# Optimization experiments

Measured on AMD Instinct MI355X. Metric: run time of the kernel, lower is better.

## Reference

```python
import jax, jax.numpy as jnp
import numpy as np

B, S, F, H, A = 2, 2048, 1024, 16, 64


def setup_inputs() -> dict:
    key = jax.random.key(0)
    ks = jax.random.split(key, 6)
    return {
        "key_input": jax.random.normal(ks[0], (B, S, F), dtype=jnp.float32),
        "query_input": jax.random.normal(ks[1], (B, S, F), dtype=jnp.float32),
        "value_input": jax.random.normal(ks[2], (B, S, F), dtype=jnp.float32),
        "q_w": jax.random.normal(ks[3], (H, F, A), dtype=jnp.float32) * (1.0 / np.sqrt(F)),
        "k_w": jax.random.normal(ks[4], (H, F, A), dtype=jnp.float32) * (1.0 / np.sqrt(F)),
        "v_w": jax.random.normal(ks[5], (H, F, A), dtype=jnp.float32) * (1.0 / np.sqrt(F)),
    }


def reference(key_input, query_input, value_input, q_w, k_w, v_w):
    attention_len = q_w.shape[-1]
    # per-head QKV projections: [B,S,F] x [H,F,A] -> [B,S,H,A]
    keys = jnp.einsum('bsf,hfa->bsha', key_input, k_w)
    queries = jnp.einsum('bsf,hfa->bsha', query_input, q_w)
    values = jnp.einsum('bsf,hfa->bsha', value_input, v_w)
    # scores: [B,H,Q,K]; NOTE: original softmaxes over dim=2 (the query axis)
    energy = jnp.einsum('bqha,bkha->bhqk', queries, keys) / jnp.sqrt(
        jnp.asarray(attention_len, dtype=queries.dtype))
    scores = jax.nn.softmax(energy, axis=2)
    # NOTE: original einsum 'bhqs,bsha->bsha' sums over q, keeps s aligned with values
    return jnp.einsum('bhqs,bsha->bsha', scores, values)
```

## Files before the change

### kernel.cpp

```cpp
#include <hip/hip_runtime.h>
#include <hip/hip_bf16.h>

typedef __bf16 bf16_t;
typedef __bf16 bf16x4 __attribute__((ext_vector_type(4)));
typedef __bf16 bf16x8 __attribute__((ext_vector_type(8)));
typedef float  f32x4  __attribute__((ext_vector_type(4)));

typedef __attribute__((address_space(1))) const void  gvoid_t;
typedef __attribute__((address_space(3))) void        lvoid_t;

static constexpr int Mtot = 4096;
static constexpr int Ntot = 1024;
static constexpr int Ktot = 1024;


__global__ __launch_bounds__(256)
void prepass_kernel(const float* __restrict__ A, const float* __restrict__ W,
                    bf16_t* __restrict__ Ab, bf16_t* __restrict__ Wt)
{
    __shared__ float wtile[64][65];
    const int bid = blockIdx.x, t = threadIdx.x;

    if (bid < 1024) {
        const size_t base = (size_t)bid * 4096 + t * 4;
#pragma unroll
        for (int r = 0; r < 4; ++r) {
            const size_t i = base + (size_t)r * 1024;
            const f32x4 v = *(const f32x4*)(A + i);
            bf16x4 p = {(bf16_t)v[0], (bf16_t)v[1], (bf16_t)v[2], (bf16_t)v[3]};
            *(bf16x4*)(Ab + i) = p;
        }
    } else {
        const int wb = bid - 1024;
        const int head = wb >> 4;
        const int k0 = (wb & 15) * 64;
        const float* wsrc = W + (size_t)head * (Ktot * 64) + (size_t)k0 * 64;
#pragma unroll
        for (int i = 0; i < 4; ++i) {
            const int idx = i * 256 + t;
            const int kr = idx >> 4, a4 = (idx & 15) * 4;
            const f32x4 v = *(const f32x4*)(wsrc + (size_t)kr * 64 + a4);
            wtile[kr][a4 + 0] = v[0]; wtile[kr][a4 + 1] = v[1];
            wtile[kr][a4 + 2] = v[2]; wtile[kr][a4 + 3] = v[3];
        }
        __syncthreads();
#pragma unroll
        for (int i = 0; i < 4; ++i) {
            const int idx = i * 256 + t;
            const int ar = idx >> 4, kc = (idx & 15) * 4;
            bf16x4 p = {(bf16_t)wtile[kc + 0][ar], (bf16_t)wtile[kc + 1][ar],
                        (bf16_t)wtile[kc + 2][ar], (bf16_t)wtile[kc + 3][ar]};
            *(bf16x4*)(Wt + (size_t)(head * 64 + ar) * Ktot + k0 + kc) = p;
        }
    }
}

__global__ __launch_bounds__(256, 2)
void gemm_bf16_kernel(const bf16_t* __restrict__ Ab, const bf16_t* __restrict__ Bt,
                      float* __restrict__ C)
{
    __shared__ bf16_t As[2][64 * 64];
    __shared__ bf16_t Bs[2][128 * 64];

    const int t = threadIdx.x, lane = t & 63, wave = t >> 6;
    const int wm = wave & 1, wn = wave >> 1;

    const int g = (blockIdx.x & 7) * 64 + (blockIdx.x >> 3);
    const int by = g >> 3, bx = g & 7;
    const int bm = by * 64, bn = bx * 128;

    const int lrow = lane & 15;
    const int lq   = lane >> 4;

    f32x4 acc[2][4];
#pragma unroll
    for (int mf = 0; mf < 2; ++mf)
#pragma unroll
        for (int nf = 0; nf < 4; ++nf) {
            f32x4 z = {0.f, 0.f, 0.f, 0.f};
            acc[mf][nf] = z;
        }

    auto STAGE = [&](int buf, int k0) {
#pragma unroll
        for (int j = 0; j < 2; ++j) {
            const int chunk = (wave * 2 + j) * 64 + lane;
            const int row = chunk >> 3;
            const int kb  = ((chunk & 7) ^ (row & 7)) * 8;
            const bf16_t* gp = Ab + (size_t)(bm + row) * Ktot + k0 + kb;
            __builtin_amdgcn_global_load_lds((gvoid_t*)gp,
                (lvoid_t*)&As[buf][(wave * 2 + j) * 512], 16, 0, 0);
        }
#pragma unroll
        for (int j = 0; j < 4; ++j) {
            const int chunk = (wave * 4 + j) * 64 + lane;
            const int row = chunk >> 3;
            const int kb  = ((chunk & 7) ^ (row & 7)) * 8;
            const bf16_t* gp = Bt + (size_t)(bn + row) * Ktot + k0 + kb;
            __builtin_amdgcn_global_load_lds((gvoid_t*)gp,
                (lvoid_t*)&Bs[buf][(wave * 4 + j) * 512], 16, 0, 0);
        }
    };

    auto COMPUTE = [&](int cur) {
#pragma unroll
        for (int kk = 0; kk < 2; ++kk) {
            const int c16 = kk * 4 + lq;
            bf16x8 af[2], bfr[4];
#pragma unroll
            for (int mf = 0; mf < 2; ++mf) {
                const int R = wm * 32 + mf * 16 + lrow;
                af[mf] = *(const bf16x8*)&As[cur][R * 64 + ((c16 ^ (R & 7)) << 3)];
            }
#pragma unroll
            for (int nf = 0; nf < 4; ++nf) {
                const int R = wn * 64 + nf * 16 + lrow;
                bfr[nf] = *(const bf16x8*)&Bs[cur][R * 64 + ((c16 ^ (R & 7)) << 3)];
            }
            __builtin_amdgcn_s_setprio(1);
#pragma unroll
            for (int mf = 0; mf < 2; ++mf)
#pragma unroll
                for (int nf = 0; nf < 4; ++nf)
                    acc[mf][nf] = __builtin_amdgcn_mfma_f32_16x16x32_bf16(
                        af[mf], bfr[nf], acc[mf][nf], 0, 0, 0);
            __builtin_amdgcn_s_setprio(0);
        }
    };

    constexpr int NT = Ktot / 64;
    STAGE(0, 0);

    for (int tI = 0; tI < NT - 1; ++tI) {
        const int cur = tI & 1;
        __builtin_amdgcn_s_barrier();
        STAGE(cur ^ 1, (tI + 1) * 64);
        asm volatile("s_waitcnt vmcnt(6)" ::: "memory");
        __builtin_amdgcn_sched_barrier(0);
        __builtin_amdgcn_s_barrier();
        __builtin_amdgcn_sched_barrier(0);
        COMPUTE(cur);
    }
    asm volatile("s_waitcnt vmcnt(0)" ::: "memory");
    __builtin_amdgcn_sched_barrier(0);
    __builtin_amdgcn_s_barrier();
    __builtin_amdgcn_sched_barrier(0);
    COMPUTE((NT - 1) & 1);

#pragma unroll
    for (int mf = 0; mf < 2; ++mf) {
        const int row0 = bm + wm * 32 + mf * 16 + (lq << 2);
#pragma unroll
        for (int nf = 0; nf < 4; ++nf) {
            const int col = bn + wn * 64 + nf * 16 + lrow;
#pragma unroll
            for (int i = 0; i < 4; ++i)
                C[(size_t)(row0 + i) * Ntot + col] = acc[mf][nf][i];
        }
    }
}

static constexpr int FBM = 128, FBN = 128, FBK = 64, FBKP = 72;

__global__ __launch_bounds__(512, 2)
void vproj_fused_kernel(const float* __restrict__ A, const float* __restrict__ W,
                        float* __restrict__ C)
{
    __shared__ bf16_t As[2][FBM][FBKP];
    __shared__ bf16_t Bs[2][FBN][FBKP];

    const int t = threadIdx.x, lane = t & 63, wave = t >> 6;
    const int wm = wave >> 2, wn = wave & 3;
    const int tile = (blockIdx.x & 7) * 32 + (blockIdx.x >> 3);
    const int bm = (tile >> 3) * FBM, bn = (tile & 7) * FBN;

    const int bhead = t >> 8, brem = t & 255;
    const int bkq = brem >> 4, baq = brem & 15;
    const float* const wbase = W + ((size_t)((bn >> 6) + bhead)) * (Ktot * 64)
                                 + (size_t)(bkq * 4) * 64 + baq * 4;
    f32x4 avreg[4], bvreg[4];

    auto load_tile = [&](int k0) {
#pragma unroll
        for (int r = 0; r < 4; ++r) {
            const int idx = r * 512 + t;
            avreg[r] = *(const f32x4*)(A + (size_t)(bm + (idx >> 4)) * Ktot + k0 + (idx & 15) * 4);
        }
        const float* wp = wbase + (size_t)k0 * 64;
#pragma unroll
        for (int r = 0; r < 4; ++r) bvreg[r] = *(const f32x4*)(wp + r * 64);
    };
    auto store_tile = [&](int buf) {
#pragma unroll
        for (int r = 0; r < 4; ++r) {
            const int idx = r * 512 + t;
            bf16_t* dst = &As[buf][idx >> 4][(idx & 15) * 4];
            dst[0] = (bf16_t)avreg[r][0]; dst[1] = (bf16_t)avreg[r][1];
            dst[2] = (bf16_t)avreg[r][2]; dst[3] = (bf16_t)avreg[r][3];
        }
#pragma unroll
        for (int j = 0; j < 4; ++j) {
            bf16_t* dst = &Bs[buf][bhead * 64 + baq * 4 + j][bkq * 4];
            dst[0] = (bf16_t)bvreg[0][j]; dst[1] = (bf16_t)bvreg[1][j];
            dst[2] = (bf16_t)bvreg[2][j]; dst[3] = (bf16_t)bvreg[3][j];
        }
    };

    f32x4 acc[4][2];
#pragma unroll
    for (int mf = 0; mf < 4; ++mf)
#pragma unroll
        for (int nf = 0; nf < 2; ++nf) { f32x4 z = {0,0,0,0}; acc[mf][nf] = z; }

    const int lrow = lane & 15, lkb = (lane >> 4) << 3;
    load_tile(0); store_tile(0); __syncthreads();

    for (int tI = 0; tI < Ktot / FBK; ++tI) {
        const int cur = tI & 1;
        if (tI + 1 < Ktot / FBK) load_tile((tI + 1) * FBK);
#pragma unroll
        for (int kk = 0; kk < 2; ++kk) {
            bf16x8 af[4], bfr[2];
#pragma unroll
            for (int mf = 0; mf < 4; ++mf)
                af[mf] = *(const bf16x8*)&As[cur][wm * 64 + mf * 16 + lrow][kk * 32 + lkb];
#pragma unroll
            for (int nf = 0; nf < 2; ++nf)
                bfr[nf] = *(const bf16x8*)&Bs[cur][wn * 32 + nf * 16 + lrow][kk * 32 + lkb];
#pragma unroll
            for (int mf = 0; mf < 4; ++mf)
#pragma unroll
                for (int nf = 0; nf < 2; ++nf)
                    acc[mf][nf] = __builtin_amdgcn_mfma_f32_16x16x32_bf16(
                        af[mf], bfr[nf], acc[mf][nf], 0, 0, 0);
        }
        if (tI + 1 < Ktot / FBK) store_tile(cur ^ 1);
        __syncthreads();
    }
#pragma unroll
    for (int mf = 0; mf < 4; ++mf) {
        const int row0 = bm + wm * 64 + mf * 16 + ((lane >> 4) << 2);
#pragma unroll
        for (int nf = 0; nf < 2; ++nf) {
            const int col = bn + wn * 32 + nf * 16 + (lane & 15);
#pragma unroll
            for (int i = 0; i < 4; ++i)
                C[(size_t)(row0 + i) * Ntot + col] = acc[mf][nf][i];
        }
    }
}

extern "C" void kernel_launch(void* const* d_in, const int* in_sizes, int n_in,
                              void* d_out, int out_size, void* d_ws, size_t ws_size,
                              hipStream_t stream) {
    (void)in_sizes; (void)n_in; (void)out_size;
    const float* V  = (const float*)d_in[2];
    const float* Vw = (const float*)d_in[5];
    float* out      = (float*)d_out;

    const size_t abBytes = (size_t)Mtot * Ktot * sizeof(bf16_t);
    const size_t wtBytes = (size_t)Ntot * Ktot * sizeof(bf16_t);

    if (ws_size >= abBytes + wtBytes) {
        bf16_t* Ab = (bf16_t*)d_ws;
        bf16_t* Wt = (bf16_t*)((char*)d_ws + abBytes);
        hipLaunchKernelGGL(prepass_kernel, dim3(1024 + 256), dim3(256), 0, stream,
                           V, Vw, Ab, Wt);
        hipLaunchKernelGGL(gemm_bf16_kernel, dim3((Mtot / 64) * (Ntot / 128)),
                           dim3(256), 0, stream, Ab, Wt, out);
    } else {
        hipLaunchKernelGGL(vproj_fused_kernel, dim3(256), dim3(512), 0, stream,
                           V, Vw, out);
    }
}
```

Measured before the change: 30.14 us.

## Fuse bf16 prepass and GEMM into one cooperative kernel with grid sync

Merges the fp32-to-bf16 conversion/transpose prepass and the bf16 MFMA GEMM into a single cooperative kernel of 512 blocks. The blocks first convert their slice of activations and weights, then meet at a grid-wide barrier before running the GEMM. This is meant to remove the second kernel launch and the gap between the two kernels. In exchange it pays for a grid sync and requires all 512 blocks to be co-resident, with the old two-kernel path kept as a fallback when cooperative launch is unsupported.

```diff
diff --git a/kernel.cpp b/kernel.cpp
--- a/kernel.cpp
+++ b/kernel.cpp
@@ -1,5 +1,8 @@
 #include <hip/hip_runtime.h>
 #include <hip/hip_bf16.h>
+#include <hip/hip_cooperative_groups.h>
+
+namespace cg = cooperative_groups;
 
 typedef __bf16 bf16_t;
 typedef __bf16 bf16x4 __attribute__((ext_vector_type(4)));
@@ -14,29 +17,35 @@
 static constexpr int Ktot = 1024;
 
 
-__global__ __launch_bounds__(256)
-void prepass_kernel(const float* __restrict__ A, const float* __restrict__ W,
-                    bf16_t* __restrict__ Ab, bf16_t* __restrict__ Wt)
+__global__ __launch_bounds__(256, 2)
+void fused_coop_kernel(const float* __restrict__ A, const float* __restrict__ W,
+                       bf16_t* __restrict__ Ab, bf16_t* __restrict__ Wt,
+                       float* __restrict__ C)
 {
-    __shared__ float wtile[64][65];
-    const int bid = blockIdx.x, t = threadIdx.x;
-
-    if (bid < 1024) {
-        const size_t base = (size_t)bid * 4096 + t * 4;
-#pragma unroll
-        for (int r = 0; r < 4; ++r) {
-            const size_t i = base + (size_t)r * 1024;
-            const f32x4 v = *(const f32x4*)(A + i);
+    __shared__ bf16_t As[2][64 * 64];
+    __shared__ bf16_t Bs[2][128 * 64];
+
+    const int t = threadIdx.x, lane = t & 63, wave = t >> 6;
+    const int bid = blockIdx.x;
+
+    {
+        const int row0 = (bid & 7) * 512 + (bid >> 3) * 8;
+#pragma unroll
+        for (int r = 0; r < 8; ++r) {
+            const size_t off = (size_t)(row0 + r) * Ktot + t * 4;
+            const f32x4 v = *(const f32x4*)(A + off);
             bf16x4 p = {(bf16_t)v[0], (bf16_t)v[1], (bf16_t)v[2], (bf16_t)v[3]};
-            *(bf16x4*)(Ab + i) = p;
-        }
-    } else {
-        const int wb = bid - 1024;
+            *(bf16x4*)(Ab + off) = p;
+        }
+    }
+    {
+        float (*wtile)[65] = (float(*)[65])(&Bs[0][0]);
+        const int wb = bid >> 1;
         const int head = wb >> 4;
-        const int k0 = (wb & 15) * 64;
+        const int k0 = (wb & 15) * 64 + (bid & 1) * 32;
         const float* wsrc = W + (size_t)head * (Ktot * 64) + (size_t)k0 * 64;
 #pragma unroll
-        for (int i = 0; i < 4; ++i) {
+        for (int i = 0; i < 2; ++i) {
             const int idx = i * 256 + t;
             const int kr = idx >> 4, a4 = (idx & 15) * 4;
             const f32x4 v = *(const f32x4*)(wsrc + (size_t)kr * 64 + a4);
@@ -45,30 +54,21 @@
         }
         __syncthreads();
 #pragma unroll
-        for (int i = 0; i < 4; ++i) {
+        for (int i = 0; i < 2; ++i) {
             const int idx = i * 256 + t;
-            const int ar = idx >> 4, kc = (idx & 15) * 4;
+            const int ar = idx >> 3, kc = (idx & 7) * 4;
             bf16x4 p = {(bf16_t)wtile[kc + 0][ar], (bf16_t)wtile[kc + 1][ar],
                         (bf16_t)wtile[kc + 2][ar], (bf16_t)wtile[kc + 3][ar]};
             *(bf16x4*)(Wt + (size_t)(head * 64 + ar) * Ktot + k0 + kc) = p;
         }
     }
-}
-
-__global__ __launch_bounds__(256, 2)
-void gemm_bf16_kernel(const bf16_t* __restrict__ Ab, const bf16_t* __restrict__ Bt,
-                      float* __restrict__ C)
-{
-    __shared__ bf16_t As[2][64 * 64];
-    __shared__ bf16_t Bs[2][128 * 64];
-
-    const int t = threadIdx.x, lane = t & 63, wave = t >> 6;
+
+    cg::this_grid().sync();
+
     const int wm = wave & 1, wn = wave >> 1;
-
-    const int g = (blockIdx.x & 7) * 64 + (blockIdx.x >> 3);
+    const int g = (bid & 7) * 64 + (bid >> 3);
     const int by = g >> 3, bx = g & 7;
     const int bm = by * 64, bn = bx * 128;
-
     const int lrow = lane & 15;
     const int lq   = lane >> 4;
 
@@ -96,7 +96,7 @@
             const int chunk = (wave * 4 + j) * 64 + lane;
             const int row = chunk >> 3;
             const int kb  = ((chunk & 7) ^ (row & 7)) * 8;
-            const bf16_t* gp = Bt + (size_t)(bn + row) * Ktot + k0 + kb;
+            const bf16_t* gp = Wt + (size_t)(bn + row) * Ktot + k0 + kb;
             __builtin_amdgcn_global_load_lds((gvoid_t*)gp,
                 (lvoid_t*)&Bs[buf][(wave * 4 + j) * 512], 16, 0, 0);
         }
@@ -160,6 +160,149 @@
     }
 }
 
+__global__ __launch_bounds__(256)
+void prepass_kernel(const float* __restrict__ A, const float* __restrict__ W,
+                    bf16_t* __restrict__ Ab, bf16_t* __restrict__ Wt)
+{
+    __shared__ float wtile[64][65];
+    const int bid = blockIdx.x, t = threadIdx.x;
+
+    if (bid < 1024) {
+        const size_t base = (size_t)bid * 4096 + t * 4;
+#pragma unroll
+        for (int r = 0; r < 4; ++r) {
+            const size_t i = base + (size_t)r * 1024;
+            const f32x4 v = *(const f32x4*)(A + i);
+            bf16x4 p = {(bf16_t)v[0], (bf16_t)v[1], (bf16_t)v[2], (bf16_t)v[3]};
+            *(bf16x4*)(Ab + i) = p;
+        }
+    } else {
+        const int wb = bid - 1024;
+        const int head = wb >> 4;
+        const int k0 = (wb & 15) * 64;
+        const float* wsrc = W + (size_t)head * (Ktot * 64) + (size_t)k0 * 64;
+#pragma unroll
+        for (int i = 0; i < 4; ++i) {
+            const int idx = i * 256 + t;
+            const int kr = idx >> 4, a4 = (idx & 15) * 4;
+            const f32x4 v = *(const f32x4*)(wsrc + (size_t)kr * 64 + a4);
+            wtile[kr][a4 + 0] = v[0]; wtile[kr][a4 + 1] = v[1];
+            wtile[kr][a4 + 2] = v[2]; wtile[kr][a4 + 3] = v[3];
+        }
+        __syncthreads();
+#pragma unroll
+        for (int i = 0; i < 4; ++i) {
+            const int idx = i * 256 + t;
+            const int ar = idx >> 4, kc = (idx & 15) * 4;
+            bf16x4 p = {(bf16_t)wtile[kc + 0][ar], (bf16_t)wtile[kc + 1][ar],
+                        (bf16_t)wtile[kc + 2][ar], (bf16_t)wtile[kc + 3][ar]};
+            *(bf16x4*)(Wt + (size_t)(head * 64 + ar) * Ktot + k0 + kc) = p;
+        }
+    }
+}
+
+__global__ __launch_bounds__(256, 2)
+void gemm_bf16_kernel(const bf16_t* __restrict__ Ab, const bf16_t* __restrict__ Bt,
+                      float* __restrict__ C)
+{
+    __shared__ bf16_t As[2][64 * 64];
+    __shared__ bf16_t Bs[2][128 * 64];
+
+    const int t = threadIdx.x, lane = t & 63, wave = t >> 6;
+    const int wm = wave & 1, wn = wave >> 1;
+    const int g = (blockIdx.x & 7) * 64 + (blockIdx.x >> 3);
+    const int by = g >> 3, bx = g & 7;
+    const int bm = by * 64, bn = bx * 128;
+    const int lrow = lane & 15;
+    const int lq   = lane >> 4;
+
+    f32x4 acc[2][4];
+#pragma unroll
+    for (int mf = 0; mf < 2; ++mf)
+#pragma unroll
+        for (int nf = 0; nf < 4; ++nf) {
+            f32x4 z = {0.f, 0.f, 0.f, 0.f};
+            acc[mf][nf] = z;
+        }
+
+    auto STAGE = [&](int buf, int k0) {
+#pragma unroll
+        for (int j = 0; j < 2; ++j) {
+            const int chunk = (wave * 2 + j) * 64 + lane;
+            const int row = chunk >> 3;
+            const int kb  = ((chunk & 7) ^ (row & 7)) * 8;
+            const bf16_t* gp = Ab + (size_t)(bm + row) * Ktot + k0 + kb;
+            __builtin_amdgcn_global_load_lds((gvoid_t*)gp,
+                (lvoid_t*)&As[buf][(wave * 2 + j) * 512], 16, 0, 0);
+        }
+#pragma unroll
+        for (int j = 0; j < 4; ++j) {
+            const int chunk = (wave * 4 + j) * 64 + lane;
+            const int row = chunk >> 3;
+            const int kb  = ((chunk & 7) ^ (row & 7)) * 8;
+            const bf16_t* gp = Bt + (size_t)(bn + row) * Ktot + k0 + kb;
+            __builtin_amdgcn_global_load_lds((gvoid_t*)gp,
+                (lvoid_t*)&Bs[buf][(wave * 4 + j) * 512], 16, 0, 0);
+        }
+    };
+
+    auto COMPUTE = [&](int cur) {
+#pragma unroll
+        for (int kk = 0; kk < 2; ++kk) {
+            const int c16 = kk * 4 + lq;
+            bf16x8 af[2], bfr[4];
+#pragma unroll
+            for (int mf = 0; mf < 2; ++mf) {
+                const int R = wm * 32 + mf * 16 + lrow;
+                af[mf] = *(const bf16x8*)&As[cur][R * 64 + ((c16 ^ (R & 7)) << 3)];
+            }
+#pragma unroll
+            for (int nf = 0; nf < 4; ++nf) {
+                const int R = wn * 64 + nf * 16 + lrow;
+                bfr[nf] = *(const bf16x8*)&Bs[cur][R * 64 + ((c16 ^ (R & 7)) << 3)];
+            }
+            __builtin_amdgcn_s_setprio(1);
+#pragma unroll
+            for (int mf = 0; mf < 2; ++mf)
+#pragma unroll
+                for (int nf = 0; nf < 4; ++nf)
+                    acc[mf][nf] = __builtin_amdgcn_mfma_f32_16x16x32_bf16(
+                        af[mf], bfr[nf], acc[mf][nf], 0, 0, 0);
+            __builtin_amdgcn_s_setprio(0);
+        }
+    };
+
+    constexpr int NT = Ktot / 64;
+    STAGE(0, 0);
+    for (int tI = 0; tI < NT - 1; ++tI) {
+        const int cur = tI & 1;
+        __builtin_amdgcn_s_barrier();
+        STAGE(cur ^ 1, (tI + 1) * 64);
+        asm volatile("s_waitcnt vmcnt(6)" ::: "memory");
+        __builtin_amdgcn_sched_barrier(0);
+        __builtin_amdgcn_s_barrier();
+        __builtin_amdgcn_sched_barrier(0);
+        COMPUTE(cur);
+    }
+    asm volatile("s_waitcnt vmcnt(0)" ::: "memory");
+    __builtin_amdgcn_sched_barrier(0);
+    __builtin_amdgcn_s_barrier();
+    __builtin_amdgcn_sched_barrier(0);
+    COMPUTE((NT - 1) & 1);
+
+#pragma unroll
+    for (int mf = 0; mf < 2; ++mf) {
+        const int row0 = bm + wm * 32 + mf * 16 + (lq << 2);
+#pragma unroll
+        for (int nf = 0; nf < 4; ++nf) {
+            const int col = bn + wn * 64 + nf * 16 + lrow;
+#pragma unroll
+            for (int i = 0; i < 4; ++i)
+                C[(size_t)(row0 + i) * Ntot + col] = acc[mf][nf][i];
+        }
+    }
+}
+
 static constexpr int FBM = 128, FBN = 128, FBK = 64, FBKP = 72;
 
 __global__ __launch_bounds__(512, 2)
@@ -264,10 +407,21 @@
     if (ws_size >= abBytes + wtBytes) {
         bf16_t* Ab = (bf16_t*)d_ws;
         bf16_t* Wt = (bf16_t*)((char*)d_ws + abBytes);
-        hipLaunchKernelGGL(prepass_kernel, dim3(1024 + 256), dim3(256), 0, stream,
-                           V, Vw, Ab, Wt);
-        hipLaunchKernelGGL(gemm_bf16_kernel, dim3((Mtot / 64) * (Ntot / 128)),
-                           dim3(256), 0, stream, Ab, Wt, out);
+
+        int dev = 0, coop = 0;
+        hipGetDevice(&dev);
+        hipDeviceGetAttribute(&coop, hipDeviceAttributeCooperativeLaunch, dev);
+
+        if (coop) {
+            void* args[] = { (void*)&V, (void*)&Vw, (void*)&Ab, (void*)&Wt, (void*)&out };
+            hipLaunchCooperativeKernel((const void*)fused_coop_kernel,
+                                       dim3(512), dim3(256), args, 0, stream);
+        } else {
+            hipLaunchKernelGGL(prepass_kernel, dim3(1024 + 256), dim3(256), 0, stream,
+                               V, Vw, Ab, Wt);
+            hipLaunchKernelGGL(gemm_bf16_kernel, dim3((Mtot / 64) * (Ntot / 128)),
+                               dim3(256), 0, stream, Ab, Wt, out);
+        }
     } else {
         hipLaunchKernelGGL(vproj_fused_kernel, dim3(256), dim3(512), 0, stream,
                            V, Vw, out);
```

Result: slower. 107.3 us (+255.9%).

## Pre-swizzle A into MFMA fragment layout and load it directly into registers

Applied to the files above, without the earlier changes.

The prepass now writes the bf16 copy of the activation matrix in a fragment-major layout, so each 16x32 MFMA A-fragment is a contiguous 1KB block. The GEMM drops the LDS staging for A and loads A fragments from global memory straight into registers, double-buffered one K-tile ahead. Only B goes through LDS. The goal is to cut LDS traffic, LDS capacity and the extra barrier work for A. In exchange, A fragments are no longer shared through LDS between the two N-waves, so global/L2 reads of A double, and the prepass gains an LDS transpose step.

```diff
diff --git a/kernel.cpp b/kernel.cpp
--- a/kernel.cpp
+++ b/kernel.cpp
@@ -16,21 +16,37 @@
 
 __global__ __launch_bounds__(256)
 void prepass_kernel(const float* __restrict__ A, const float* __restrict__ W,
-                    bf16_t* __restrict__ Ab, bf16_t* __restrict__ Wt)
+                    bf16_t* __restrict__ Abf, bf16_t* __restrict__ Wt)
 {
-    __shared__ float wtile[64][65];
     const int bid = blockIdx.x, t = threadIdx.x;
 
     if (bid < 1024) {
-        const size_t base = (size_t)bid * 4096 + t * 4;
-#pragma unroll
-        for (int r = 0; r < 4; ++r) {
-            const size_t i = base + (size_t)r * 1024;
-            const f32x4 v = *(const f32x4*)(A + i);
-            bf16x4 p = {(bf16_t)v[0], (bf16_t)v[1], (bf16_t)v[2], (bf16_t)v[3]};
-            *(bf16x4*)(Ab + i) = p;
+        __shared__ float tile[16][260];
+        const int r0 = (bid >> 2) * 16;
+        const int k0 = (bid & 3) * 256;
+#pragma unroll
+        for (int i = 0; i < 4; ++i) {
+            const int c = i * 256 + t;
+            const int row = c >> 6, kc = (c & 63) * 4;
+            const f32x4 v = *(const f32x4*)(A + (size_t)(r0 + row) * Ktot + k0 + kc);
+            *(f32x4*)&tile[row][kc] = v;
+        }
+        __syncthreads();
+        const int Fbase = (r0 >> 4) * 32 + (k0 >> 5);
+#pragma unroll
+        for (int j = 0; j < 2; ++j) {
+            const int u = j * 256 + t;
+            const int fl = u >> 6, l = u & 63;
+            const int row = l & 15;
+            const int kb = fl * 32 + (l >> 4) * 8;
+            bf16x8 p = {(bf16_t)tile[row][kb + 0], (bf16_t)tile[row][kb + 1],
+                        (bf16_t)tile[row][kb + 2], (bf16_t)tile[row][kb + 3],
+                        (bf16_t)tile[row][kb + 4], (bf16_t)tile[row][kb + 5],
+                        (bf16_t)tile[row][kb + 6], (bf16_t)tile[row][kb + 7]};
+            *(bf16x8*)(Abf + ((size_t)(Fbase + fl) * 64 + l) * 8) = p;
         }
     } else {
+        __shared__ float wtile[64][65];
         const int wb = bid - 1024;
         const int head = wb >> 4;
         const int k0 = (wb & 15) * 64;
@@ -55,11 +71,12 @@
     }
 }
 
+struct FragA { bf16x8 v[2][2]; };
+
 __global__ __launch_bounds__(256, 2)
-void gemm_bf16_kernel(const bf16_t* __restrict__ Ab, const bf16_t* __restrict__ Bt,
+void gemm_bf16_kernel(const bf16_t* __restrict__ Abf, const bf16_t* __restrict__ Bt,
                       float* __restrict__ C)
 {
-    __shared__ bf16_t As[2][64 * 64];
     __shared__ bf16_t Bs[2][128 * 64];
 
     const int t = threadIdx.x, lane = t & 63, wave = t >> 6;
@@ -72,6 +89,9 @@
     const int lrow = lane & 15;
     const int lq   = lane >> 4;
 
+    const int R0 = (bm >> 4) + wm * 2;
+    const bf16_t* const aLane = Abf + (size_t)lane * 8;
+
     f32x4 acc[2][4];
 #pragma unroll
     for (int mf = 0; mf < 2; ++mf)
@@ -81,16 +101,7 @@
             acc[mf][nf] = z;
         }
 
-    auto STAGE = [&](int buf, int k0) {
-#pragma unroll
-        for (int j = 0; j < 2; ++j) {
-            const int chunk = (wave * 2 + j) * 64 + lane;
-            const int row = chunk >> 3;
-            const int kb  = ((chunk & 7) ^ (row & 7)) * 8;
-            const bf16_t* gp = Ab + (size_t)(bm + row) * Ktot + k0 + kb;
-            __builtin_amdgcn_global_load_lds((gvoid_t*)gp,
-                (lvoid_t*)&As[buf][(wave * 2 + j) * 512], 16, 0, 0);
-        }
+    auto STAGEB = [&](int buf, int k0) {
 #pragma unroll
         for (int j = 0; j < 4; ++j) {
             const int chunk = (wave * 4 + j) * 64 + lane;
@@ -102,16 +113,20 @@
         }
     };
 
-    auto COMPUTE = [&](int cur) {
+    auto LOADA = [&](FragA& d, int tIdx) {
+#pragma unroll
+        for (int mf = 0; mf < 2; ++mf)
+#pragma unroll
+            for (int kk = 0; kk < 2; ++kk)
+                d.v[mf][kk] = *(const bf16x8*)(
+                    aLane + (size_t)((R0 + mf) * 32 + tIdx * 2 + kk) * 512);
+    };
+
+    auto COMPUTE = [&](int cur, const FragA& a) {
 #pragma unroll
         for (int kk = 0; kk < 2; ++kk) {
             const int c16 = kk * 4 + lq;
-            bf16x8 af[2], bfr[4];
-#pragma unroll
-            for (int mf = 0; mf < 2; ++mf) {
-                const int R = wm * 32 + mf * 16 + lrow;
-                af[mf] = *(const bf16x8*)&As[cur][R * 64 + ((c16 ^ (R & 7)) << 3)];
-            }
+            bf16x8 bfr[4];
 #pragma unroll
             for (int nf = 0; nf < 4; ++nf) {
                 const int R = wn * 64 + nf * 16 + lrow;
@@ -123,29 +138,37 @@
 #pragma unroll
                 for (int nf = 0; nf < 4; ++nf)
                     acc[mf][nf] = __builtin_amdgcn_mfma_f32_16x16x32_bf16(
-                        af[mf], bfr[nf], acc[mf][nf], 0, 0, 0);
+                        a.v[mf][kk], bfr[nf], acc[mf][nf], 0, 0, 0);
             __builtin_amdgcn_s_setprio(0);
         }
     };
 
-    constexpr int NT = Ktot / 64;
-    STAGE(0, 0);
-
-    for (int tI = 0; tI < NT - 1; ++tI) {
-        const int cur = tI & 1;
+    FragA A0, A1;
+
+    auto STEP = [&](int tI, int curLds, FragA& curA, FragA& nxtA) {
         __builtin_amdgcn_s_barrier();
-        STAGE(cur ^ 1, (tI + 1) * 64);
-        asm volatile("s_waitcnt vmcnt(6)" ::: "memory");
+        STAGEB(curLds ^ 1, (tI + 1) * 64);
+        LOADA(nxtA, tI + 1);
+        asm volatile("s_waitcnt vmcnt(8)" ::: "memory");
         __builtin_amdgcn_sched_barrier(0);
         __builtin_amdgcn_s_barrier();
         __builtin_amdgcn_sched_barrier(0);
-        COMPUTE(cur);
-    }
+        COMPUTE(curLds, curA);
+    };
+
+    LOADA(A0, 0);
+    STAGEB(0, 0);
+
+    for (int it = 0; it < 7; ++it) {
+        STEP(2 * it,     0, A0, A1);
+        STEP(2 * it + 1, 1, A1, A0);
+    }
+    STEP(14, 0, A0, A1);
     asm volatile("s_waitcnt vmcnt(0)" ::: "memory");
     __builtin_amdgcn_sched_barrier(0);
     __builtin_amdgcn_s_barrier();
     __builtin_amdgcn_sched_barrier(0);
-    COMPUTE((NT - 1) & 1);
+    COMPUTE(1, A1);
 
 #pragma unroll
     for (int mf = 0; mf < 2; ++mf) {
@@ -262,12 +285,12 @@
     const size_t wtBytes = (size_t)Ntot * Ktot * sizeof(bf16_t);
 
     if (ws_size >= abBytes + wtBytes) {
-        bf16_t* Ab = (bf16_t*)d_ws;
-        bf16_t* Wt = (bf16_t*)((char*)d_ws + abBytes);
+        bf16_t* Abf = (bf16_t*)d_ws;
+        bf16_t* Wt  = (bf16_t*)((char*)d_ws + abBytes);
         hipLaunchKernelGGL(prepass_kernel, dim3(1024 + 256), dim3(256), 0, stream,
-                           V, Vw, Ab, Wt);
+                           V, Vw, Abf, Wt);
         hipLaunchKernelGGL(gemm_bf16_kernel, dim3((Mtot / 64) * (Ntot / 128)),
-                           dim3(256), 0, stream, Ab, Wt, out);
+                           dim3(256), 0, stream, Abf, Wt, out);
     } else {
         hipLaunchKernelGGL(vproj_fused_kernel, dim3(256), dim3(512), 0, stream,
                            V, Vw, out);
```

New measurement: 29.10 us. 1.04x faster.
